# Kernel optimization log

Hardware: AMD Instinct MI355X
Metric: run time of the kernel (lower is better)

The kernel has to match this reference:

```python
import jax, jax.numpy as jnp
import numpy as np

N_NODES = 50000
DROP_P = 0.2


def gcn_conv(x, edge_index, W, b):
    """PyG GCNConv: add self-loops, symmetric D^-1/2 (A+I) D^-1/2 normalization."""
    n = x.shape[0]
    loop = jnp.arange(n, dtype=edge_index.dtype)
    src = jnp.concatenate([edge_index[0], loop])  # [E+N]
    dst = jnp.concatenate([edge_index[1], loop])  # [E+N]
    # degree over destination (incl. self loop), all edge weights = 1
    deg = jax.ops.segment_sum(jnp.ones_like(src, dtype=x.dtype), dst, num_segments=n)
    dinv = jnp.where(deg > 0, jax.lax.rsqrt(deg), 0.0)
    norm = dinv[src] * dinv[dst]  # [E+N]
    h = x @ W  # [N, F_out] transform first (PyG order)
    msg = h[src] * norm[:, None]  # gather + scale
    out = jax.ops.segment_sum(msg, dst, num_segments=n)  # scatter-add
    return out + b


def setup_inputs() -> dict:
    key = jax.random.key(0)
    ks = jax.random.split(key, 4)
    x = jax.random.normal(ks[0], (N_NODES, 512), dtype=jnp.float32)
    edge_index = jax.random.randint(ks[1], (2, 800000), 0, N_NODES, dtype=jnp.int64)
    W1 = jax.random.normal(ks[2], (512, 256), dtype=jnp.float32) * (1.0 / np.sqrt(512))
    b1 = jnp.zeros((256,), dtype=jnp.float32)
    W2 = jax.random.normal(ks[3], (256, 128), dtype=jnp.float32) * (1.0 / np.sqrt(256))
    b2 = jnp.zeros((128,), dtype=jnp.float32)
    return {"x": x, "edge_index": edge_index, "W1": W1, "b1": b1, "W2": W2, "b2": b2}


def reference(x, edge_index, W1, b1, W2, b2):
    h = gcn_conv(x, edge_index, W1, b1)
    h = jax.nn.relu(h)
    # F.dropout(p=0.2) with training=True default; deterministic fixed-key mask
    keep = jax.random.bernoulli(jax.random.key(42), 1.0 - DROP_P, h.shape)
    h = jnp.where(keep, h / (1.0 - DROP_P), 0.0)
    h = gcn_conv(h, edge_index, W2, b2)
    return jax.nn.softmax(h, axis=1)
```

## Files before the change

### kernel.cpp

```cpp
#include <hip/hip_runtime.h>
#include <stdint.h>

#define N_NODES 50000
#define N_EDGES 800000
#define F0 512
#define F1 256
#define F2 128
#define CAP 64

typedef __attribute__((ext_vector_type(8))) short short8;
typedef __attribute__((ext_vector_type(4))) float float4v;

__device__ __forceinline__ uint32_t r8_rotl(uint32_t x, int r) {
    return (x << r) | (x >> (32 - r));
}

__device__ __forceinline__ uint32_t r8_bits32(uint32_t idx) {
    const uint32_t ks0 = 0u;
    const uint32_t ks1 = 42u;
    const uint32_t ks2 = 0x1BD11BDAu ^ ks0 ^ ks1;
    uint32_t x0 = ks0;
    uint32_t x1 = idx + ks1;
#define R8R(r) { x0 += x1; x1 = r8_rotl(x1, (r)); x1 ^= x0; }
    R8R(13) R8R(15) R8R(26) R8R(6)
    x0 += ks1; x1 += ks2 + 1u;
    R8R(17) R8R(29) R8R(16) R8R(24)
    x0 += ks2; x1 += ks0 + 2u;
    R8R(13) R8R(15) R8R(26) R8R(6)
    x0 += ks0; x1 += ks1 + 3u;
    R8R(17) R8R(29) R8R(16) R8R(24)
    x0 += ks1; x1 += ks2 + 4u;
    R8R(13) R8R(15) R8R(26) R8R(6)
    x0 += ks2; x1 += ks0 + 5u;
#undef R8R
    return x0 ^ x1;
}

__device__ __forceinline__ int r8_keep(uint32_t idx) {
    return (r8_bits32(idx) >> 9) < 0x666667u;
}

__device__ __forceinline__ unsigned short r8_f2bf(float f) {
    uint32_t u = __float_as_uint(f);
    uint32_t r = u + 0x7fffu + ((u >> 16) & 1u);
    return (unsigned short)(r >> 16);
}

__global__ void r8_zero(int* __restrict__ p, int n) {
    int i = blockIdx.x * 256 + threadIdx.x;
    if (i < n) p[i] = 0;
}

__global__ void r8_detect(const uint32_t* __restrict__ ei, int* __restrict__ flag) {
    int t = threadIdx.x;
    uint32_t v = ei[2 * t + 1] | ei[128 + 2 * t + 1];
    unsigned long long any_nonzero = __ballot(v != 0u);
    if (t == 0) flag[0] = (any_nonzero == 0ull) ? 1 : 0;
}

__global__ void r8_fill(const int* __restrict__ ei, const int* __restrict__ flag,
                        int* __restrict__ cursor, int* __restrict__ bucket) {
    int e = blockIdx.x * 256 + threadIdx.x;
    if (e < N_EDGES) {
        int f = flag[0];
        int s = ei[(size_t)e << f];
        int d = ei[(size_t)(N_EDGES + e) << f];
        int pos = atomicAdd(&cursor[d], 1);
        if (pos < CAP) bucket[(size_t)d * CAP + pos] = s;
    }
}

__global__ void r8_dinv(const int* __restrict__ cursor, float* __restrict__ dinv) {
    int v = blockIdx.x * 256 + threadIdx.x;
    if (v < N_NODES) dinv[v] = 1.0f / sqrtf((float)(cursor[v] + 1));
}

__global__ void r8_w1t(const float* __restrict__ W1, unsigned short* __restrict__ Bt) {
    int k = blockIdx.x;
    int n = threadIdx.x;
    Bt[(size_t)n * F0 + k] = r8_f2bf(W1[(size_t)k * F1 + n]);
}

#define G1_LDA 40
__global__ __launch_bounds__(256)
void r8_gemm1(const float* __restrict__ A, const unsigned short* __restrict__ Bt,
              unsigned short* __restrict__ C, int M) {
    __shared__ unsigned short As[128][G1_LDA];
    __shared__ unsigned short Bs[128][G1_LDA];
    const int bm = blockIdx.x * 128;
    const int bn = blockIdx.y * 128;
    const int tid = threadIdx.x;
    const int wave = tid >> 6;
    const int lane = tid & 63;
    const int wm = (wave & 1) * 64;
    const int wn = (wave >> 1) * 64;
    const int l15 = lane & 15;
    const int quad = lane >> 4;

    const int sr = tid >> 1;
    const int sk = (tid & 1) * 16;

    float4v acc[4][4];
#pragma unroll
    for (int i = 0; i < 4; ++i)
#pragma unroll
        for (int j = 0; j < 4; ++j) acc[i][j] = (float4v){0.f, 0.f, 0.f, 0.f};

    const int arow = bm + sr;
    const bool avalid = arow < M;
    const float* aptr = A + (size_t)(avalid ? arow : 0) * F0 + sk;
    const unsigned short* bptr = Bt + (size_t)(bn + sr) * F0 + sk;

    for (int k0 = 0; k0 < F0; k0 += 32) {
        union { short8 v[2]; unsigned short u[16]; } at;
        if (avalid) {
            const float4* ap = (const float4*)(aptr + k0);
#pragma unroll
            for (int q = 0; q < 4; ++q) {
                float4 f = ap[q];
                at.u[q * 4 + 0] = r8_f2bf(f.x);
                at.u[q * 4 + 1] = r8_f2bf(f.y);
                at.u[q * 4 + 2] = r8_f2bf(f.z);
                at.u[q * 4 + 3] = r8_f2bf(f.w);
            }
        } else {
#pragma unroll
            for (int q = 0; q < 16; ++q) at.u[q] = 0;
        }
        *(short8*)&As[sr][sk] = at.v[0];
        *(short8*)&As[sr][sk + 8] = at.v[1];
        *(short8*)&Bs[sr][sk] = *(const short8*)(bptr + k0);
        *(short8*)&Bs[sr][sk + 8] = *(const short8*)(bptr + k0 + 8);
        __syncthreads();

        short8 afr[4], bfr[4];
#pragma unroll
        for (int mi = 0; mi < 4; ++mi)
            afr[mi] = *(const short8*)&As[wm + mi * 16 + l15][quad * 8];
#pragma unroll
        for (int ni = 0; ni < 4; ++ni)
            bfr[ni] = *(const short8*)&Bs[wn + ni * 16 + l15][quad * 8];
#pragma unroll
        for (int mi = 0; mi < 4; ++mi)
#pragma unroll
            for (int ni = 0; ni < 4; ++ni)
                acc[mi][ni] = __builtin_amdgcn_mfma_f32_16x16x32_bf16(
                    afr[mi], bfr[ni], acc[mi][ni], 0, 0, 0);
        __syncthreads();
    }

#pragma unroll
    for (int mi = 0; mi < 4; ++mi) {
#pragma unroll
        for (int r = 0; r < 4; ++r) {
            int row = bm + wm + mi * 16 + quad * 4 + r;
            if (row < M) {
                unsigned short* cp = C + (size_t)row * F1 + bn + wn + l15;
#pragma unroll
                for (int ni = 0; ni < 4; ++ni) cp[ni * 16] = r8_f2bf(acc[mi][ni][r]);
            }
        }
    }
}

__global__ __launch_bounds__(256)
void r8_sgemm(const float* __restrict__ A, const float* __restrict__ B,
              unsigned short* __restrict__ C, int M, int N, int K) {
    __shared__ float As[16][64];
    __shared__ float Bs[16][64];
    const int bm = blockIdx.x * 64;
    const int bn = blockIdx.y * 64;
    const int tid = threadIdx.x;
    const int tr = (tid >> 4) << 2;
    const int tc = (tid & 15) << 2;
    const int arow = tid >> 2;
    const int acol = (tid & 3) << 2;
    const int brow = tid >> 4;
    const int bcol = (tid & 15) << 2;

    float acc[4][4] = {{0.f}};
    for (int k0 = 0; k0 < K; k0 += 16) {
        float4 av = make_float4(0.f, 0.f, 0.f, 0.f);
        if (bm + arow < M)
            av = *(const float4*)(A + (size_t)(bm + arow) * K + (k0 + acol));
        As[acol + 0][arow] = av.x;
        As[acol + 1][arow] = av.y;
        As[acol + 2][arow] = av.z;
        As[acol + 3][arow] = av.w;
        *(float4*)&Bs[brow][bcol] =
            *(const float4*)(B + (size_t)(k0 + brow) * N + (bn + bcol));
        __syncthreads();
#pragma unroll
        for (int kk = 0; kk < 16; ++kk) {
            float4 a = *(const float4*)&As[kk][tr];
            float4 b = *(const float4*)&Bs[kk][tc];
            acc[0][0] += a.x * b.x; acc[0][1] += a.x * b.y; acc[0][2] += a.x * b.z; acc[0][3] += a.x * b.w;
            acc[1][0] += a.y * b.x; acc[1][1] += a.y * b.y; acc[1][2] += a.y * b.z; acc[1][3] += a.y * b.w;
            acc[2][0] += a.z * b.x; acc[2][1] += a.z * b.y; acc[2][2] += a.z * b.z; acc[2][3] += a.z * b.w;
            acc[3][0] += a.w * b.x; acc[3][1] += a.w * b.y; acc[3][2] += a.w * b.z; acc[3][3] += a.w * b.w;
        }
        __syncthreads();
    }
#pragma unroll
    for (int i = 0; i < 4; ++i) {
        int row = bm + tr + i;
        if (row < M) {
            uint2 st;
            st.x = (uint32_t)r8_f2bf(acc[i][0]) | ((uint32_t)r8_f2bf(acc[i][1]) << 16);
            st.y = (uint32_t)r8_f2bf(acc[i][2]) | ((uint32_t)r8_f2bf(acc[i][3]) << 16);
            *(uint2*)(C + (size_t)row * N + bn + tc) = st;
        }
    }
}

__global__ __launch_bounds__(256)
void r8_prop1(const unsigned short* __restrict__ h1, const int* __restrict__ bucket,
              const int* __restrict__ deg, const float* __restrict__ dinv,
              const float* __restrict__ b1, float* __restrict__ a1) {
    const int v = (blockIdx.x << 2) + (threadIdx.x >> 6);
    const int lane = threadIdx.x & 63;
    const float dv = dinv[v];
    int cnt = deg[v]; if (cnt > CAP) cnt = CAP;

    int s_l = 0; float w_l = 0.f;
    if (lane < cnt) {
        s_l = bucket[(size_t)v * CAP + lane];
        w_l = dinv[s_l] * dv;
    }

    const unsigned short* hrow = h1 + (size_t)lane * 4;
    uint2 hq = *(const uint2*)(h1 + (size_t)v * F1 + lane * 4);
    const float w0 = dv * dv;
    float ax = __uint_as_float(hq.x << 16) * w0;
    float ay = __uint_as_float(hq.x & 0xffff0000u) * w0;
    float az = __uint_as_float(hq.y << 16) * w0;
    float aw = __uint_as_float(hq.y & 0xffff0000u) * w0;

    for (int j = 0; j < cnt; j += 8) {
        int   s[8];
        float w[8];
#pragma unroll
        for (int u = 0; u < 8; ++u) {
            s[u] = __shfl(s_l, j + u);
            w[u] = __shfl(w_l, j + u);
        }
        uint2 r[8];
#pragma unroll
        for (int u = 0; u < 8; ++u)
            r[u] = *(const uint2*)(hrow + (size_t)s[u] * F1);
#pragma unroll
        for (int u = 0; u < 8; ++u) {
            ax += __uint_as_float(r[u].x << 16) * w[u];
            ay += __uint_as_float(r[u].x & 0xffff0000u) * w[u];
            az += __uint_as_float(r[u].y << 16) * w[u];
            aw += __uint_as_float(r[u].y & 0xffff0000u) * w[u];
        }
    }

    float4 bb = *(const float4*)(b1 + lane * 4);
    ax = fmaxf(ax + bb.x, 0.f);
    ay = fmaxf(ay + bb.y, 0.f);
    az = fmaxf(az + bb.z, 0.f);
    aw = fmaxf(aw + bb.w, 0.f);
    uint32_t idx = (uint32_t)v * F1 + (uint32_t)lane * 4;
    float4 rr;
    rr.x = r8_keep(idx + 0) ? ax * 1.25f : 0.0f;
    rr.y = r8_keep(idx + 1) ? ay * 1.25f : 0.0f;
    rr.z = r8_keep(idx + 2) ? az * 1.25f : 0.0f;
    rr.w = r8_keep(idx + 3) ? aw * 1.25f : 0.0f;
    *(float4*)(a1 + (size_t)v * F1 + lane * 4) = rr;
}

__global__ __launch_bounds__(256)
void r8_prop2(const unsigned short* __restrict__ h2, const int* __restrict__ bucket,
              const int* __restrict__ deg, const float* __restrict__ dinv,
              const float* __restrict__ b2, float* __restrict__ out) {
    const int v = (blockIdx.x << 2) + (threadIdx.x >> 6);
    const int lane = threadIdx.x & 63;
    const float dv = dinv[v];
    int cnt = deg[v]; if (cnt > CAP) cnt = CAP;

    int s_l = 0; float w_l = 0.f;
    if (lane < cnt) {
        s_l = bucket[(size_t)v * CAP + lane];
        w_l = dinv[s_l] * dv;
    }

    const unsigned short* hrow = h2 + (size_t)lane * 2;
    uint32_t hq = *(const uint32_t*)(h2 + (size_t)v * F2 + lane * 2);
    const float w0 = dv * dv;
    float ax = __uint_as_float(hq << 16) * w0;
    float ay = __uint_as_float(hq & 0xffff0000u) * w0;

    for (int j = 0; j < cnt; j += 8) {
        int   s[8];
        float w[8];
#pragma unroll
        for (int u = 0; u < 8; ++u) {
            s[u] = __shfl(s_l, j + u);
            w[u] = __shfl(w_l, j + u);
        }
        uint32_t r[8];
#pragma unroll
        for (int u = 0; u < 8; ++u)
            r[u] = *(const uint32_t*)(hrow + (size_t)s[u] * F2);
#pragma unroll
        for (int u = 0; u < 8; ++u) {
            ax += __uint_as_float(r[u] << 16) * w[u];
            ay += __uint_as_float(r[u] & 0xffff0000u) * w[u];
        }
    }

    float2 bb = *(const float2*)(b2 + lane * 2);
    ax += bb.x; ay += bb.y;
    float m = fmaxf(ax, ay);
#pragma unroll
    for (int o = 32; o >= 1; o >>= 1) m = fmaxf(m, __shfl_xor(m, o, 64));
    float ex = expf(ax - m), ey = expf(ay - m);
    float s = ex + ey;
#pragma unroll
    for (int o = 32; o >= 1; o >>= 1) s += __shfl_xor(s, o, 64);
    float inv = 1.0f / s;
    *(float2*)(out + (size_t)v * F2 + lane * 2) = make_float2(ex * inv, ey * inv);
}

extern "C" void kernel_launch(void* const* d_in, const int* in_sizes, int n_in,
                              void* d_out, int out_size, void* d_ws, size_t ws_size,
                              hipStream_t stream) {
    const float* x  = (const float*)d_in[0];
    const int*   ei = (const int*)d_in[1];
    const float* W1 = (const float*)d_in[2];
    const float* b1 = (const float*)d_in[3];
    const float* W2 = (const float*)d_in[4];
    const float* b2 = (const float*)d_in[5];
    float* out = (float*)d_out;

    char* ws = (char*)d_ws;
    size_t o = 0;
    auto alloc = [&](size_t bytes) -> char* {
        char* p = ws + o;
        o += (bytes + 511) & ~(size_t)511;
        return p;
    };
    int*            flag   = (int*)           alloc(4);
    int*            cursor = (int*)           alloc((size_t)N_NODES * 4);
    float*          dinv   = (float*)         alloc((size_t)N_NODES * 4);
    int*            bucket = (int*)           alloc((size_t)N_NODES * CAP * 4);
    unsigned short* w1t    = (unsigned short*)alloc((size_t)F1 * F0 * 2);
    unsigned short* h1     = (unsigned short*)alloc((size_t)N_NODES * F1 * 2);
    float*          a1     = (float*)         alloc((size_t)N_NODES * F1 * 4);
    unsigned short* h2     = (unsigned short*)alloc((size_t)N_NODES * F2 * 2);

    r8_zero<<<(N_NODES + 255) / 256, 256, 0, stream>>>(cursor, N_NODES);
    r8_detect<<<1, 64, 0, stream>>>((const uint32_t*)ei, flag);
    r8_fill<<<(N_EDGES + 255) / 256, 256, 0, stream>>>(ei, flag, cursor, bucket);
    r8_dinv<<<(N_NODES + 255) / 256, 256, 0, stream>>>(cursor, dinv);
    r8_w1t<<<F0, F1, 0, stream>>>(W1, w1t);

    dim3 g1((N_NODES + 127) / 128, F1 / 128);
    r8_gemm1<<<g1, 256, 0, stream>>>(x, w1t, h1, N_NODES);

    r8_prop1<<<N_NODES / 4, 256, 0, stream>>>(h1, bucket, cursor, dinv, b1, a1);

    dim3 g2((N_NODES + 63) / 64, F2 / 64);
    r8_sgemm<<<g2, 256, 0, stream>>>(a1, W2, h2, N_NODES, F2, F1);

    r8_prop2<<<N_NODES / 4, 256, 0, stream>>>(h2, bucket, cursor, dinv, b2, out);
}
```

Measured before the change: 392.2 us.

## Use bf16 MFMA for second GEMM, store a1 as bf16, double-buffer GEMM1

The second layer's fp32 SIMT GEMM becomes a bf16 MFMA GEMM that reads a transposed bf16 copy of W2, and prop1 now writes its output as bf16 instead of fp32. GEMM1 gains register-prefetched double-buffered shared memory, and its grid is reordered so blocks sharing the same A rows run next to each other. The aim is to cut GEMM2 compute time and the memory traffic of the intermediate activations. The cost is extra rounding error from storing activations in bf16 and more shared memory per block.

```diff
diff --git a/kernel.cpp b/kernel.cpp
--- a/kernel.cpp
+++ b/kernel.cpp
@@ -81,14 +81,20 @@
     Bt[(size_t)n * F0 + k] = r8_f2bf(W1[(size_t)k * F1 + n]);
 }
 
+__global__ void r8_w2t(const float* __restrict__ W2, unsigned short* __restrict__ Bt) {
+    int k = blockIdx.x;
+    int n = threadIdx.x;
+    Bt[(size_t)n * F1 + k] = r8_f2bf(W2[(size_t)k * F2 + n]);
+}
+
 #define G1_LDA 40
 __global__ __launch_bounds__(256)
 void r8_gemm1(const float* __restrict__ A, const unsigned short* __restrict__ Bt,
               unsigned short* __restrict__ C, int M) {
-    __shared__ unsigned short As[128][G1_LDA];
-    __shared__ unsigned short Bs[128][G1_LDA];
-    const int bm = blockIdx.x * 128;
-    const int bn = blockIdx.y * 128;
+    __shared__ unsigned short As[2][128][G1_LDA];
+    __shared__ unsigned short Bs[2][128][G1_LDA];
+    const int bn = blockIdx.x * 128;
+    const int bm = blockIdx.y * 128;
     const int tid = threadIdx.x;
     const int wave = tid >> 6;
     const int lane = tid & 63;
@@ -111,41 +117,63 @@
     const float* aptr = A + (size_t)(avalid ? arow : 0) * F0 + sk;
     const unsigned short* bptr = Bt + (size_t)(bn + sr) * F0 + sk;
 
-    for (int k0 = 0; k0 < F0; k0 += 32) {
+    float4 apf[4];
+#pragma unroll
+    for (int q = 0; q < 4; ++q) apf[q] = make_float4(0.f, 0.f, 0.f, 0.f);
+    short8 bpf[2];
+
+    if (avalid) {
+        const float4* ap = (const float4*)aptr;
+#pragma unroll
+        for (int q = 0; q < 4; ++q) apf[q] = ap[q];
+    }
+    bpf[0] = *(const short8*)(bptr);
+    bpf[1] = *(const short8*)(bptr + 8);
+
+    auto write_buf = [&](int buf) {
         union { short8 v[2]; unsigned short u[16]; } at;
-        if (avalid) {
-            const float4* ap = (const float4*)(aptr + k0);
-#pragma unroll
-            for (int q = 0; q < 4; ++q) {
-                float4 f = ap[q];
-                at.u[q * 4 + 0] = r8_f2bf(f.x);
-                at.u[q * 4 + 1] = r8_f2bf(f.y);
-                at.u[q * 4 + 2] = r8_f2bf(f.z);
-                at.u[q * 4 + 3] = r8_f2bf(f.w);
+#pragma unroll
+        for (int q = 0; q < 4; ++q) {
+            at.u[q * 4 + 0] = r8_f2bf(apf[q].x);
+            at.u[q * 4 + 1] = r8_f2bf(apf[q].y);
+            at.u[q * 4 + 2] = r8_f2bf(apf[q].z);
+            at.u[q * 4 + 3] = r8_f2bf(apf[q].w);
+        }
+        *(short8*)&As[buf][sr][sk] = at.v[0];
+        *(short8*)&As[buf][sr][sk + 8] = at.v[1];
+        *(short8*)&Bs[buf][sr][sk] = bpf[0];
+        *(short8*)&Bs[buf][sr][sk + 8] = bpf[1];
+    };
+    write_buf(0);
+    __syncthreads();
+
+    const int NT = F0 / 32;
+    for (int kt = 0; kt < NT; ++kt) {
+        const int cur = kt & 1;
+        if (kt + 1 < NT) {
+            const int k0 = (kt + 1) * 32;
+            if (avalid) {
+                const float4* ap = (const float4*)(aptr + k0);
+#pragma unroll
+                for (int q = 0; q < 4; ++q) apf[q] = ap[q];
             }
-        } else {
-#pragma unroll
-            for (int q = 0; q < 16; ++q) at.u[q] = 0;
-        }
-        *(short8*)&As[sr][sk] = at.v[0];
-        *(short8*)&As[sr][sk + 8] = at.v[1];
-        *(short8*)&Bs[sr][sk] = *(const short8*)(bptr + k0);
-        *(short8*)&Bs[sr][sk + 8] = *(const short8*)(bptr + k0 + 8);
-        __syncthreads();
-
+            bpf[0] = *(const short8*)(bptr + k0);
+            bpf[1] = *(const short8*)(bptr + k0 + 8);
+        }
         short8 afr[4], bfr[4];
 #pragma unroll
         for (int mi = 0; mi < 4; ++mi)
-            afr[mi] = *(const short8*)&As[wm + mi * 16 + l15][quad * 8];
+            afr[mi] = *(const short8*)&As[cur][wm + mi * 16 + l15][quad * 8];
 #pragma unroll
         for (int ni = 0; ni < 4; ++ni)
-            bfr[ni] = *(const short8*)&Bs[wn + ni * 16 + l15][quad * 8];
+            bfr[ni] = *(const short8*)&Bs[cur][wn + ni * 16 + l15][quad * 8];
 #pragma unroll
         for (int mi = 0; mi < 4; ++mi)
 #pragma unroll
             for (int ni = 0; ni < 4; ++ni)
                 acc[mi][ni] = __builtin_amdgcn_mfma_f32_16x16x32_bf16(
                     afr[mi], bfr[ni], acc[mi][ni], 0, 0, 0);
+        if (kt + 1 < NT) write_buf(cur ^ 1);
         __syncthreads();
     }
 
@@ -163,52 +191,88 @@
     }
 }
 
+#define G2_LDA 40
 __global__ __launch_bounds__(256)
-void r8_sgemm(const float* __restrict__ A, const float* __restrict__ B,
-              unsigned short* __restrict__ C, int M, int N, int K) {
-    __shared__ float As[16][64];
-    __shared__ float Bs[16][64];
+void r8_gemm2(const unsigned short* __restrict__ A, const unsigned short* __restrict__ Bt,
+              unsigned short* __restrict__ C, int M) {
+    __shared__ unsigned short As[2][64][G2_LDA];
+    __shared__ unsigned short Bs[2][128][G2_LDA];
     const int bm = blockIdx.x * 64;
-    const int bn = blockIdx.y * 64;
     const int tid = threadIdx.x;
-    const int tr = (tid >> 4) << 2;
-    const int tc = (tid & 15) << 2;
-    const int arow = tid >> 2;
-    const int acol = (tid & 3) << 2;
-    const int brow = tid >> 4;
-    const int bcol = (tid & 15) << 2;
-
-    float acc[4][4] = {{0.f}};
-    for (int k0 = 0; k0 < K; k0 += 16) {
-        float4 av = make_float4(0.f, 0.f, 0.f, 0.f);
-        if (bm + arow < M)
-            av = *(const float4*)(A + (size_t)(bm + arow) * K + (k0 + acol));
-        As[acol + 0][arow] = av.x;
-        As[acol + 1][arow] = av.y;
-        As[acol + 2][arow] = av.z;
-        As[acol + 3][arow] = av.w;
-        *(float4*)&Bs[brow][bcol] =
-            *(const float4*)(B + (size_t)(k0 + brow) * N + (bn + bcol));
+    const int wave = tid >> 6;
+    const int lane = tid & 63;
+    const int wm = (wave & 1) * 32;
+    const int wn = (wave >> 1) * 64;
+    const int l15 = lane & 15;
+    const int quad = lane >> 4;
+
+    const int asr = tid >> 2;
+    const int ask = (tid & 3) * 8;
+    const int bsr = tid >> 1;
+    const int bsk = (tid & 1) * 16;
+
+    float4v acc[2][4];
+#pragma unroll
+    for (int i = 0; i < 2; ++i)
+#pragma unroll
+        for (int j = 0; j < 4; ++j) acc[i][j] = (float4v){0.f, 0.f, 0.f, 0.f};
+
+    const int arow = bm + asr;
+    const bool avalid = arow < M;
+    const unsigned short* aptr = A + (size_t)(avalid ? arow : 0) * F1 + ask;
+    const unsigned short* bptr = Bt + (size_t)bsr * F1 + bsk;
+
+    short8 apf = (short8){0, 0, 0, 0, 0, 0, 0, 0};
+    short8 bpf[2];
+
+    if (avalid) apf = *(const short8*)aptr;
+    bpf[0] = *(const short8*)(bptr);
+    bpf[1] = *(const short8*)(bptr + 8);
+
+    auto write_buf = [&](int buf) {
+        *(short8*)&As[buf][asr][ask] = apf;
+        *(short8*)&Bs[buf][bsr][bsk] = bpf[0];
+        *(short8*)&Bs[buf][bsr][bsk + 8] = bpf[1];
+    };
+    write_buf(0);
+    __syncthreads();
+
+    const int NT = F1 / 32;
+    for (int kt = 0; kt < NT; ++kt) {
+        const int cur = kt & 1;
+        if (kt + 1 < NT) {
+            const int k0 = (kt + 1) * 32;
+            if (avalid) apf = *(const short8*)(aptr + k0);
+            bpf[0] = *(const short8*)(bptr + k0);
+            bpf[1] = *(const short8*)(bptr + k0 + 8);
+        }
+        short8 afr[2], bfr[4];
+#pragma unroll
+        for (int mi = 0; mi < 2; ++mi)
+            afr[mi] = *(const short8*)&As[cur][wm + mi * 16 + l15][quad * 8];
+#pragma unroll
+        for (int ni = 0; ni < 4; ++ni)
+            bfr[ni] = *(const short8*)&Bs[cur][wn + ni * 16 + l15][quad * 8];
+#pragma unroll
+        for (int mi = 0; mi < 2; ++mi)
+#pragma unroll
+            for (int ni = 0; ni < 4; ++ni)
+                acc[mi][ni] = __builtin_amdgcn_mfma_f32_16x16x32_bf16(
+                    afr[mi], bfr[ni], acc[mi][ni], 0, 0, 0);
+        if (kt + 1 < NT) write_buf(cur ^ 1);
         __syncthreads();
-#pragma unroll
-        for (int kk = 0; kk < 16; ++kk) {
-            float4 a = *(const float4*)&As[kk][tr];
-            float4 b = *(const float4*)&Bs[kk][tc];
-            acc[0][0] += a.x * b.x; acc[0][1] += a.x * b.y; acc[0][2] += a.x * b.z; acc[0][3] += a.x * b.w;
-            acc[1][0] += a.y * b.x; acc[1][1] += a.y * b.y; acc[1][2] += a.y * b.z; acc[1][3] += a.y * b.w;
-            acc[2][0] += a.z * b.x; acc[2][1] += a.z * b.y; acc[2][2] += a.z * b.z; acc[2][3] += a.z * b.w;
-            acc[3][0] += a.w * b.x; acc[3][1] += a.w * b.y; acc[3][2] += a.w * b.z; acc[3][3] += a.w * b.w;
-        }
-        __syncthreads();
-    }
-#pragma unroll
-    for (int i = 0; i < 4; ++i) {
-        int row = bm + tr + i;
-        if (row < M) {
-            uint2 st;
-            st.x = (uint32_t)r8_f2bf(acc[i][0]) | ((uint32_t)r8_f2bf(acc[i][1]) << 16);
-            st.y = (uint32_t)r8_f2bf(acc[i][2]) | ((uint32_t)r8_f2bf(acc[i][3]) << 16);
-            *(uint2*)(C + (size_t)row * N + bn + tc) = st;
+    }
+
+#pragma unroll
+    for (int mi = 0; mi < 2; ++mi) {
+#pragma unroll
+        for (int r = 0; r < 4; ++r) {
+            int row = bm + wm + mi * 16 + quad * 4 + r;
+            if (row < M) {
+                unsigned short* cp = C + (size_t)row * F2 + wn + l15;
+#pragma unroll
+                for (int ni = 0; ni < 4; ++ni) cp[ni * 16] = r8_f2bf(acc[mi][ni][r]);
+            }
         }
     }
 }
@@ -216,7 +280,7 @@
 __global__ __launch_bounds__(256)
 void r8_prop1(const unsigned short* __restrict__ h1, const int* __restrict__ bucket,
               const int* __restrict__ deg, const float* __restrict__ dinv,
-              const float* __restrict__ b1, float* __restrict__ a1) {
+              const float* __restrict__ b1, unsigned short* __restrict__ a1) {
     const int v = (blockIdx.x << 2) + (threadIdx.x >> 6);
     const int lane = threadIdx.x & 63;
     const float dv = dinv[v];
@@ -263,12 +327,14 @@
     az = fmaxf(az + bb.z, 0.f);
     aw = fmaxf(aw + bb.w, 0.f);
     uint32_t idx = (uint32_t)v * F1 + (uint32_t)lane * 4;
-    float4 rr;
-    rr.x = r8_keep(idx + 0) ? ax * 1.25f : 0.0f;
-    rr.y = r8_keep(idx + 1) ? ay * 1.25f : 0.0f;
-    rr.z = r8_keep(idx + 2) ? az * 1.25f : 0.0f;
-    rr.w = r8_keep(idx + 3) ? aw * 1.25f : 0.0f;
-    *(float4*)(a1 + (size_t)v * F1 + lane * 4) = rr;
+    ax = r8_keep(idx + 0) ? ax * 1.25f : 0.0f;
+    ay = r8_keep(idx + 1) ? ay * 1.25f : 0.0f;
+    az = r8_keep(idx + 2) ? az * 1.25f : 0.0f;
+    aw = r8_keep(idx + 3) ? aw * 1.25f : 0.0f;
+    uint2 st;
+    st.x = (uint32_t)r8_f2bf(ax) | ((uint32_t)r8_f2bf(ay) << 16);
+    st.y = (uint32_t)r8_f2bf(az) | ((uint32_t)r8_f2bf(aw) << 16);
+    *(uint2*)(a1 + (size_t)v * F1 + lane * 4) = st;
 }
 
 __global__ __launch_bounds__(256)
@@ -347,8 +413,9 @@
     float*          dinv   = (float*)         alloc((size_t)N_NODES * 4);
     int*            bucket = (int*)           alloc((size_t)N_NODES * CAP * 4);
     unsigned short* w1t    = (unsigned short*)alloc((size_t)F1 * F0 * 2);
+    unsigned short* w2t    = (unsigned short*)alloc((size_t)F2 * F1 * 2);
     unsigned short* h1     = (unsigned short*)alloc((size_t)N_NODES * F1 * 2);
-    float*          a1     = (float*)         alloc((size_t)N_NODES * F1 * 4);
+    unsigned short* a1     = (unsigned short*)alloc((size_t)N_NODES * F1 * 2);
     unsigned short* h2     = (unsigned short*)alloc((size_t)N_NODES * F2 * 2);
 
     r8_zero<<<(N_NODES + 255) / 256, 256, 0, stream>>>(cursor, N_NODES);
@@ -356,14 +423,14 @@
     r8_fill<<<(N_EDGES + 255) / 256, 256, 0, stream>>>(ei, flag, cursor, bucket);
     r8_dinv<<<(N_NODES + 255) / 256, 256, 0, stream>>>(cursor, dinv);
     r8_w1t<<<F0, F1, 0, stream>>>(W1, w1t);
-
-    dim3 g1((N_NODES + 127) / 128, F1 / 128);
+    r8_w2t<<<F1, F2, 0, stream>>>(W2, w2t);
+
+    dim3 g1(F1 / 128, (N_NODES + 127) / 128);
     r8_gemm1<<<g1, 256, 0, stream>>>(x, w1t, h1, N_NODES);
 
     r8_prop1<<<N_NODES / 4, 256, 0, stream>>>(h1, bucket, cursor, dinv, b1, a1);
 
-    dim3 g2((N_NODES + 63) / 64, F2 / 64);
-    r8_sgemm<<<g2, 256, 0, stream>>>(a1, W2, h2, N_NODES, F2, F1);
+    r8_gemm2<<<(N_NODES + 63) / 64, 256, 0, stream>>>(a1, w2t, h2, N_NODES);
 
     r8_prop2<<<N_NODES / 4, 256, 0, stream>>>(h2, bucket, cursor, dinv, b2, out);
 }
```

Result: faster. 353.3 us (-9.9%).
